# Performance work log

Measured on AMD Instinct MI355X. Metric: run time of the kernel, lower is better.

The kernel has to match this reference:

```python
import jax, jax.numpy as jnp
import numpy as np

B, T, C = 4, 2048, 1024
NH = 16
HD = C // NH  # 64

def setup_inputs() -> dict:
    key = jax.random.key(0)
    k1, k2, k3 = jax.random.split(key, 3)
    x = jax.random.normal(k1, (B, T, C), dtype=jnp.float32)
    w_qkv = jax.random.normal(k2, (C, 3 * C), dtype=jnp.float32) * (1.0 / np.sqrt(C))
    w_out = jax.random.normal(k3, (C, C), dtype=jnp.float32) * (1.0 / np.sqrt(C))
    b_out = jnp.zeros((C,), dtype=jnp.float32)
    return {"x": x, "w_qkv": w_qkv, "w_out": w_out, "b_out": b_out}

def reference(x, w_qkv, w_out, b_out):
    b, t, c = x.shape
    nh, hd = NH, c // NH
    qkv = x @ w_qkv                      # [b, t, 3c]
    q, k, v = jnp.split(qkv, 3, axis=-1)
    # [b, t, c] -> [b, nh, t, hd]
    def heads(z):
        return z.reshape(b, t, nh, hd).transpose(0, 2, 1, 3)
    q, k, v = heads(q), heads(k), heads(v)
    scale = 1.0 / jnp.sqrt(jnp.asarray(hd, dtype=x.dtype))
    scores = jnp.einsum('bhqd,bhkd->bhqk', q, k) * scale  # [b, nh, t, t]
    causal = jnp.tril(jnp.ones((t, t), dtype=bool))
    scores = jnp.where(causal, scores, jnp.asarray(-jnp.inf, dtype=scores.dtype))
    attn = jax.nn.softmax(scores, axis=-1)
    ctx = jnp.einsum('bhqk,bhkd->bhqd', attn, v)           # [b, nh, t, hd]
    ctx = ctx.transpose(0, 2, 1, 3).reshape(b, t, c)
    return ctx @ w_out + b_out
```

## Files before the change

### kernel.cpp

```cpp
#include <hip/hip_runtime.h>
#include <cmath>


typedef __bf16 bf16x4 __attribute__((ext_vector_type(4)));
typedef __bf16 bf16x8 __attribute__((ext_vector_type(8)));
typedef float  f32x4  __attribute__((ext_vector_type(4)));

__device__ __forceinline__ void gload_lds16(const __bf16* g, __bf16* l) {
    __builtin_amdgcn_global_load_lds(
        (const __attribute__((address_space(1))) void*)g,
        (__attribute__((address_space(3))) void*)l,
        16, 0, 0);
}

__global__ __launch_bounds__(256) void cast_bf16(const float* __restrict__ in,
                                                 __bf16* __restrict__ out, int n4) {
    int i = blockIdx.x * 256 + threadIdx.x;
    if (i >= n4) return;
    float4 f = *(const float4*)(in + (size_t)i * 4);
    bf16x4 o;
    o[0] = (__bf16)f.x; o[1] = (__bf16)f.y; o[2] = (__bf16)f.z; o[3] = (__bf16)f.w;
    *(bf16x4*)(out + (size_t)i * 4) = o;
}

__global__ __launch_bounds__(256) void transpose_cast(const float* __restrict__ W,
                                                      __bf16* __restrict__ WT,
                                                      int K, int N) {
    __shared__ float tile[32][33];
    const int n0 = blockIdx.x * 32, k0 = blockIdx.y * 32;
    const int tx = threadIdx.x & 31, ty = threadIdx.x >> 5;
    #pragma unroll
    for (int i = 0; i < 4; ++i)
        tile[ty + 8 * i][tx] = W[(size_t)(k0 + ty + 8 * i) * N + n0 + tx];
    __syncthreads();
    #pragma unroll
    for (int i = 0; i < 4; ++i)
        WT[(size_t)(n0 + ty + 8 * i) * K + k0 + tx] = (__bf16)tile[tx][ty + 8 * i];
}

__global__ __launch_bounds__(256) void transpose_v(const __bf16* __restrict__ qkv,
                                                   __bf16* __restrict__ Vt) {
    constexpr int T = 2048, R3C = 3072;
    __shared__ __bf16 tile[64][72];
    const int bh = blockIdx.y;
    const int b  = bh >> 4, h = bh & 15;
    const int kt = blockIdx.x * 64;
    const int tid = threadIdx.x;
    #pragma unroll
    for (int i = 0; i < 2; ++i) {
        int idx = tid + 256 * i;
        int kr  = idx >> 3;
        int c8  = idx & 7;
        *(uint4*)&tile[kr][c8 * 8] =
            *(const uint4*)(qkv + (size_t)(b * T + kt + kr) * R3C + 2048 + h * 64 + c8 * 8);
    }
    __syncthreads();
    #pragma unroll
    for (int i = 0; i < 2; ++i) {
        int idx = tid + 256 * i;
        int d   = idx >> 3;
        int k8  = idx & 7;
        union { __bf16 v[8]; uint4 u; } t;
        #pragma unroll
        for (int j = 0; j < 8; ++j) t.v[j] = tile[k8 * 8 + j][d];
        *(uint4*)(Vt + ((size_t)bh * 64 + d) * T + kt + k8 * 8) = t.u;
    }
}

template <typename OutT, bool BIAS>
__global__ __launch_bounds__(256) void gemm_bt(const __bf16* __restrict__ A,
                                               const __bf16* __restrict__ BT,
                                               OutT* __restrict__ Cc,
                                               const float* __restrict__ bias,
                                               int M, int N, int K) {
    __shared__ __bf16 As[128 * 32];
    __shared__ __bf16 Bs[128 * 32];

    const int tid  = threadIdx.x;
    const int lane = tid & 63;
    const int w    = tid >> 6;
    const int wr   = w >> 1, wc = w & 1;
    const int cc   = lane & 15, gg = lane >> 4;
    const int rowBase = blockIdx.y * 128;
    const int colBase = blockIdx.x * 128;

    f32x4 acc[4][4];
    #pragma unroll
    for (int i = 0; i < 4; ++i)
        #pragma unroll
        for (int j = 0; j < 4; ++j) acc[i][j] = f32x4{0.f, 0.f, 0.f, 0.f};

    for (int k0 = 0; k0 < K; k0 += 32) {
        __syncthreads();
        #pragma unroll
        for (int i = 0; i < 2; ++i) {
            int idx = tid + 256 * i;
            int r   = idx >> 2;
            int c4  = idx & 3;
            gload_lds16(A  + (size_t)(rowBase + r) * K + k0 + c4 * 8, &As[idx * 8]);
            gload_lds16(BT + (size_t)(colBase + r) * K + k0 + c4 * 8, &Bs[idx * 8]);
        }
        __syncthreads();

        bf16x8 af[4], bfr[4];
        #pragma unroll
        for (int i = 0; i < 4; ++i)
            af[i] = *(const bf16x8*)&As[(wr * 64 + i * 16 + cc) * 32 + gg * 8];
        #pragma unroll
        for (int j = 0; j < 4; ++j)
            bfr[j] = *(const bf16x8*)&Bs[(wc * 64 + j * 16 + cc) * 32 + gg * 8];
        #pragma unroll
        for (int i = 0; i < 4; ++i)
            #pragma unroll
            for (int j = 0; j < 4; ++j)
                acc[i][j] = __builtin_amdgcn_mfma_f32_16x16x32_bf16(af[i], bfr[j], acc[i][j], 0, 0, 0);
    }

    #pragma unroll
    for (int i = 0; i < 4; ++i)
        #pragma unroll
        for (int j = 0; j < 4; ++j) {
            const int col = colBase + wc * 64 + j * 16 + cc;
            #pragma unroll
            for (int r = 0; r < 4; ++r) {
                const int row = rowBase + wr * 64 + i * 16 + gg * 4 + r;
                float v = acc[i][j][r];
                if (BIAS) v += bias[col];
                Cc[(size_t)row * N + col] = (OutT)v;
            }
        }
}

__global__ __launch_bounds__(256) void flash_attn_mfma(const __bf16* __restrict__ qkv,
                                                       const __bf16* __restrict__ Vt,
                                                       __bf16* __restrict__ ctx) {
    constexpr int T = 2048, C = 1024, NH = 16, HD = 64;
    constexpr int R3C = 3 * C;
    constexpr float K1 = 0.125f * 1.44269504088896f;
    constexpr float K2 = -16.0f * 1.44269504088896f;

    const int tid  = threadIdx.x;
    const int lane = tid & 63;
    const int w    = tid >> 6;
    const int c    = lane & 15;
    const int g    = lane >> 4;

    const int bh    = blockIdx.x;
    const int qt    = 15 - (int)blockIdx.y;
    const int b     = bh >> 4;
    const int h     = bh & 15;
    const int qbase = qt * 128;

    __shared__ __attribute__((aligned(16))) __bf16 Ks [64][72];
    __shared__ __attribute__((aligned(16))) __bf16 VsT[64][72];
    __shared__ __attribute__((aligned(16))) __bf16 Ps [4][32][72];

    const __bf16* Qhead = qkv + (size_t)(b * T) * R3C + h * HD;
    bf16x8 Qa[2][2];
    #pragma unroll
    for (int st = 0; st < 2; ++st)
        #pragma unroll
        for (int ks = 0; ks < 2; ++ks)
            Qa[st][ks] = *(const bf16x8*)(Qhead +
                (size_t)(qbase + w * 32 + st * 16 + c) * R3C + ks * 32 + g * 8);

    f32x4 O0[4], O1[4];
    #pragma unroll
    for (int n = 0; n < 4; ++n) { O0[n] = f32x4{0.f,0.f,0.f,0.f}; O1[n] = f32x4{0.f,0.f,0.f,0.f}; }
    float l0[4] = {0.f,0.f,0.f,0.f}, l1[4] = {0.f,0.f,0.f,0.f};

    const __bf16* Kb  = qkv + (size_t)(b * T) * R3C + C + h * HD;
    const __bf16* Vtb = Vt + (size_t)bh * 64 * T;

    const int srow0 = qbase + w * 32;
    const int srow1 = srow0 + 16;
    const int ktmax = qbase + 64;

    for (int kt = 0; kt <= ktmax; kt += 64) {
        __syncthreads();
        #pragma unroll
        for (int i = 0; i < 2; ++i) {
            int idx = tid + 256 * i;
            int kr  = idx >> 3;
            int c8  = idx & 7;
            *(uint4*)&Ks[kr][c8 * 8] = *(const uint4*)(Kb + (size_t)(kt + kr) * R3C + c8 * 8);
        }
        #pragma unroll
        for (int i = 0; i < 2; ++i) {
            int idx = tid + 256 * i;
            int d   = idx >> 3;
            int k8  = idx & 7;
            *(uint4*)&VsT[d][k8 * 8] = *(const uint4*)(Vtb + (size_t)d * T + kt + k8 * 8);
        }
        __syncthreads();

        f32x4 S0[4], S1[4];
        #pragma unroll
        for (int s = 0; s < 4; ++s) { S0[s] = f32x4{0.f,0.f,0.f,0.f}; S1[s] = f32x4{0.f,0.f,0.f,0.f}; }
        #pragma unroll
        for (int ks = 0; ks < 2; ++ks)
            #pragma unroll
            for (int sub = 0; sub < 4; ++sub) {
                bf16x8 kb = *(const bf16x8*)&Ks[sub * 16 + c][ks * 32 + g * 8];
                S0[sub] = __builtin_amdgcn_mfma_f32_16x16x32_bf16(Qa[0][ks], kb, S0[sub], 0, 0, 0);
                S1[sub] = __builtin_amdgcn_mfma_f32_16x16x32_bf16(Qa[1][ks], kb, S1[sub], 0, 0, 0);
            }
        if (kt + 63 > srow0) {
            #pragma unroll
            for (int sub = 0; sub < 4; ++sub) {
                int key = kt + sub * 16 + c;
                #pragma unroll
                for (int r = 0; r < 4; ++r)
                    if (key > srow0 + g * 4 + r) S0[sub][r] = -1e30f;
            }
        }
        if (kt + 63 > srow1) {
            #pragma unroll
            for (int sub = 0; sub < 4; ++sub) {
                int key = kt + sub * 16 + c;
                #pragma unroll
                for (int r = 0; r < 4; ++r)
                    if (key > srow1 + g * 4 + r) S1[sub][r] = -1e30f;
            }
        }
        #pragma unroll
        for (int sub = 0; sub < 4; ++sub)
            #pragma unroll
            for (int r = 0; r < 4; ++r) {
                float p0 = exp2f(fmaf(S0[sub][r], K1, K2));
                float p1 = exp2f(fmaf(S1[sub][r], K1, K2));
                l0[r] += p0; l1[r] += p1;
                Ps[w][g * 4 + r]     [sub * 16 + c] = (__bf16)p0;
                Ps[w][16 + g * 4 + r][sub * 16 + c] = (__bf16)p1;
            }

        #pragma unroll
        for (int ks = 0; ks < 2; ++ks) {
            bf16x8 pa0 = *(const bf16x8*)&Ps[w][c]     [ks * 32 + g * 8];
            bf16x8 pa1 = *(const bf16x8*)&Ps[w][16 + c][ks * 32 + g * 8];
            #pragma unroll
            for (int n = 0; n < 4; ++n) {
                bf16x8 vb = *(const bf16x8*)&VsT[n * 16 + c][ks * 32 + g * 8];
                O0[n] = __builtin_amdgcn_mfma_f32_16x16x32_bf16(pa0, vb, O0[n], 0, 0, 0);
                O1[n] = __builtin_amdgcn_mfma_f32_16x16x32_bf16(pa1, vb, O1[n], 0, 0, 0);
            }
        }
    }

    #pragma unroll
    for (int off = 1; off <= 8; off <<= 1)
        #pragma unroll
        for (int r = 0; r < 4; ++r) {
            l0[r] += __shfl_xor(l0[r], off);
            l1[r] += __shfl_xor(l1[r], off);
        }

    #pragma unroll
    for (int r = 0; r < 4; ++r) { l0[r] = 1.f / l0[r]; l1[r] = 1.f / l1[r]; }
    #pragma unroll
    for (int n = 0; n < 4; ++n)
        #pragma unroll
        for (int r = 0; r < 4; ++r) {
            size_t row0 = (size_t)(b * T + srow0 + g * 4 + r);
            size_t row1 = (size_t)(b * T + srow1 + g * 4 + r);
            ctx[row0 * C + h * HD + n * 16 + c] = (__bf16)(O0[n][r] * l0[r]);
            ctx[row1 * C + h * HD + n * 16 + c] = (__bf16)(O1[n][r] * l1[r]);
        }
}

extern "C" void kernel_launch(void* const* d_in, const int* in_sizes, int n_in,
                              void* d_out, int out_size, void* d_ws, size_t ws_size,
                              hipStream_t stream) {
    constexpr int B = 4, T = 2048, C = 1024;
    constexpr int M = B * T;

    const float* x     = (const float*)d_in[0];
    const float* w_qkv = (const float*)d_in[1];
    const float* w_out = (const float*)d_in[2];
    const float* b_out = (const float*)d_in[3];
    float* out = (float*)d_out;

    char* ws = (char*)d_ws;
    __bf16* xb     = (__bf16*)(ws);
    __bf16* wqkvT  = (__bf16*)(ws + (16ull << 20));
    __bf16* woutT  = (__bf16*)(ws + (22ull << 20));
    __bf16* qkvb   = (__bf16*)(ws + (24ull << 20));
    __bf16* ctxb   = (__bf16*)(ws + (72ull << 20));
    __bf16* Vt     = (__bf16*)(ws + (88ull << 20));

    cast_bf16<<<(M * C / 4 + 255) / 256, 256, 0, stream>>>(x, xb, M * C / 4);
    transpose_cast<<<dim3(3 * C / 32, C / 32), 256, 0, stream>>>(w_qkv, wqkvT, C, 3 * C);
    transpose_cast<<<dim3(C / 32, C / 32), 256, 0, stream>>>(w_out, woutT, C, C);

    gemm_bt<__bf16, false><<<dim3(3 * C / 128, M / 128), 256, 0, stream>>>(
        xb, wqkvT, qkvb, nullptr, M, 3 * C, C);

    transpose_v<<<dim3(T / 64, B * 16), 256, 0, stream>>>(qkvb, Vt);

    flash_attn_mfma<<<dim3(B * 16, T / 128), 256, 0, stream>>>(qkvb, Vt, ctxb);

    gemm_bt<float, true><<<dim3(C / 128, M / 128), 256, 0, stream>>>(
        ctxb, woutT, out, b_out, M, C, C);
}
```

Before: 291.1 us.

## Prefetch K/V tiles into registers and compute softmax row sums via MFMA

Flash attention now loads the next K and V^T tile into registers while the current tile is being computed, so global-load latency overlaps with the MFMA work. The per-lane scalar row-sum accumulation and the cross-lane shuffle reduction are replaced by an extra MFMA against a ones vector. The sum now comes from the bf16-rounded P, so it matches the numerator. Launch bounds add a minimum of 4 blocks per SM to cap register use, which risks spills given the extra prefetch registers.

New measurement: 331.7 us. 1.14x slower.

```diff
diff --git a/kernel.cpp b/kernel.cpp
--- a/kernel.cpp
+++ b/kernel.cpp
@@ -131,9 +131,9 @@
         }
 }
 
-__global__ __launch_bounds__(256) void flash_attn_mfma(const __bf16* __restrict__ qkv,
-                                                       const __bf16* __restrict__ Vt,
-                                                       __bf16* __restrict__ ctx) {
+__global__ __launch_bounds__(256, 4) void flash_attn_mfma(const __bf16* __restrict__ qkv,
+                                                          const __bf16* __restrict__ Vt,
+                                                          __bf16* __restrict__ ctx) {
     constexpr int T = 2048, C = 1024, NH = 16, HD = 64;
     constexpr int R3C = 3 * C;
     constexpr float K1 = 0.125f * 1.44269504088896f;
@@ -164,10 +164,14 @@
             Qa[st][ks] = *(const bf16x8*)(Qhead +
                 (size_t)(qbase + w * 32 + st * 16 + c) * R3C + ks * 32 + g * 8);
 
-    f32x4 O0[4], O1[4];
+    f32x4 O0[4], O1[4], L0, L1;
     #pragma unroll
     for (int n = 0; n < 4; ++n) { O0[n] = f32x4{0.f,0.f,0.f,0.f}; O1[n] = f32x4{0.f,0.f,0.f,0.f}; }
-    float l0[4] = {0.f,0.f,0.f,0.f}, l1[4] = {0.f,0.f,0.f,0.f};
+    L0 = f32x4{0.f,0.f,0.f,0.f}; L1 = f32x4{0.f,0.f,0.f,0.f};
+
+    bf16x8 ones;
+    #pragma unroll
+    for (int j = 0; j < 8; ++j) ones[j] = (__bf16)1.0f;
 
     const __bf16* Kb  = qkv + (size_t)(b * T) * R3C + C + h * HD;
     const __bf16* Vtb = Vt + (size_t)bh * 64 * T;
@@ -176,23 +180,29 @@
     const int srow1 = srow0 + 16;
     const int ktmax = qbase + 64;
 
+    const int krA = tid >> 3,        c8A = tid & 7;
+    const int krB = (tid + 256) >> 3, c8B = tid & 7;
+
+    uint4 kreg0 = *(const uint4*)(Kb + (size_t)krA * R3C + c8A * 8);
+    uint4 kreg1 = *(const uint4*)(Kb + (size_t)krB * R3C + c8B * 8);
+    uint4 vreg0 = *(const uint4*)(Vtb + (size_t)krA * T + c8A * 8);
+    uint4 vreg1 = *(const uint4*)(Vtb + (size_t)krB * T + c8B * 8);
+
     for (int kt = 0; kt <= ktmax; kt += 64) {
         __syncthreads();
-        #pragma unroll
-        for (int i = 0; i < 2; ++i) {
-            int idx = tid + 256 * i;
-            int kr  = idx >> 3;
-            int c8  = idx & 7;
-            *(uint4*)&Ks[kr][c8 * 8] = *(const uint4*)(Kb + (size_t)(kt + kr) * R3C + c8 * 8);
-        }
-        #pragma unroll
-        for (int i = 0; i < 2; ++i) {
-            int idx = tid + 256 * i;
-            int d   = idx >> 3;
-            int k8  = idx & 7;
-            *(uint4*)&VsT[d][k8 * 8] = *(const uint4*)(Vtb + (size_t)d * T + kt + k8 * 8);
-        }
+        *(uint4*)&Ks [krA][c8A * 8] = kreg0;
+        *(uint4*)&Ks [krB][c8B * 8] = kreg1;
+        *(uint4*)&VsT[krA][c8A * 8] = vreg0;
+        *(uint4*)&VsT[krB][c8B * 8] = vreg1;
         __syncthreads();
+
+        if (kt + 64 <= ktmax) {
+            const __bf16* Kn = Kb + (size_t)(kt + 64) * R3C;
+            kreg0 = *(const uint4*)(Kn + (size_t)krA * R3C + c8A * 8);
+            kreg1 = *(const uint4*)(Kn + (size_t)krB * R3C + c8B * 8);
+            vreg0 = *(const uint4*)(Vtb + (size_t)krA * T + kt + 64 + c8A * 8);
+            vreg1 = *(const uint4*)(Vtb + (size_t)krB * T + kt + 64 + c8B * 8);
+        }
 
         f32x4 S0[4], S1[4];
         #pragma unroll
@@ -229,7 +239,6 @@
             for (int r = 0; r < 4; ++r) {
                 float p0 = exp2f(fmaf(S0[sub][r], K1, K2));
                 float p1 = exp2f(fmaf(S1[sub][r], K1, K2));
-                l0[r] += p0; l1[r] += p1;
                 Ps[w][g * 4 + r]     [sub * 16 + c] = (__bf16)p0;
                 Ps[w][16 + g * 4 + r][sub * 16 + c] = (__bf16)p1;
             }
@@ -244,27 +253,22 @@
                 O0[n] = __builtin_amdgcn_mfma_f32_16x16x32_bf16(pa0, vb, O0[n], 0, 0, 0);
                 O1[n] = __builtin_amdgcn_mfma_f32_16x16x32_bf16(pa1, vb, O1[n], 0, 0, 0);
             }
+            L0 = __builtin_amdgcn_mfma_f32_16x16x32_bf16(pa0, ones, L0, 0, 0, 0);
+            L1 = __builtin_amdgcn_mfma_f32_16x16x32_bf16(pa1, ones, L1, 0, 0, 0);
         }
     }
 
-    #pragma unroll
-    for (int off = 1; off <= 8; off <<= 1)
-        #pragma unroll
-        for (int r = 0; r < 4; ++r) {
-            l0[r] += __shfl_xor(l0[r], off);
-            l1[r] += __shfl_xor(l1[r], off);
-        }
-
-    #pragma unroll
-    for (int r = 0; r < 4; ++r) { l0[r] = 1.f / l0[r]; l1[r] = 1.f / l1[r]; }
+    float i0[4], i1[4];
+    #pragma unroll
+    for (int r = 0; r < 4; ++r) { i0[r] = 1.f / L0[r]; i1[r] = 1.f / L1[r]; }
     #pragma unroll
     for (int n = 0; n < 4; ++n)
         #pragma unroll
         for (int r = 0; r < 4; ++r) {
             size_t row0 = (size_t)(b * T + srow0 + g * 4 + r);
             size_t row1 = (size_t)(b * T + srow1 + g * 4 + r);
-            ctx[row0 * C + h * HD + n * 16 + c] = (__bf16)(O0[n][r] * l0[r]);
-            ctx[row1 * C + h * HD + n * 16 + c] = (__bf16)(O1[n][r] * l1[r]);
+            ctx[row0 * C + h * HD + n * 16 + c] = (__bf16)(O0[n][r] * i0[r]);
+            ctx[row1 * C + h * HD + n * 16 + c] = (__bf16)(O1[n][r] * i1[r]);
         }
 }
 
```
